# Optimization experiments

Hardware: AMD Instinct MI355X
Metric: run time of the kernel (lower is better)

## Reference

```python
import jax, jax.numpy as jnp
import numpy as np
from jax import lax

INPUT_DIM = 16
H1, H2 = 64, 32
OUT_DIM = 1
B, T = 4096, 168


def _uniform(key, shape, k):
    return jax.random.uniform(key, shape, jnp.float32, -k, k)


def setup_inputs() -> dict:
    key = jax.random.key(0)
    ks = jax.random.split(key, 12)
    k1 = 1.0 / np.sqrt(H1)
    k2 = 1.0 / np.sqrt(H2)
    return {
        "x": jax.random.normal(ks[0], (B, T, INPUT_DIM), jnp.float32),
        # layer 1 (PyTorch gate order: i, f, g, o)
        "W_ih1": _uniform(ks[1], (4 * H1, INPUT_DIM), k1),
        "W_hh1": _uniform(ks[2], (4 * H1, H1), k1),
        "b_ih1": _uniform(ks[3], (4 * H1,), k1),
        "b_hh1": _uniform(ks[4], (4 * H1,), k1),
        # layer 2
        "W_ih2": _uniform(ks[5], (4 * H2, H1), k2),
        "W_hh2": _uniform(ks[6], (4 * H2, H2), k2),
        "b_ih2": _uniform(ks[7], (4 * H2,), k2),
        "b_hh2": _uniform(ks[8], (4 * H2,), k2),
        # final linear
        "W_fc": _uniform(ks[9], (OUT_DIM, H2), k2),
        "b_fc": _uniform(ks[10], (OUT_DIM,), k2),
    }


def _lstm(x, W_ih, W_hh, b_ih, b_hh, hidden):
    # Precompute input-to-gate projections for all timesteps: [B, T, 4H]
    xg = jnp.einsum("btd,gd->btg", x, W_ih) + b_ih + b_hh

    def step(carry, xt):
        h, c = carry
        gates = xt + h @ W_hh.T  # [B, 4H]
        i, f, g, o = jnp.split(gates, 4, axis=-1)
        i = jax.nn.sigmoid(i)
        f = jax.nn.sigmoid(f)
        g = jnp.tanh(g)
        o = jax.nn.sigmoid(o)
        c = f * c + i * g
        h = o * jnp.tanh(c)
        return (h, c), h

    bsz = x.shape[0]
    init = (jnp.zeros((bsz, hidden), x.dtype), jnp.zeros((bsz, hidden), x.dtype))
    (_, _), hs = lax.scan(step, init, jnp.swapaxes(xg, 0, 1))  # hs: [T, B, H]
    return jnp.swapaxes(hs, 0, 1)  # [B, T, H]


def reference(x, W_ih1, W_hh1, b_ih1, b_hh1, W_ih2, W_hh2, b_ih2, b_hh2, W_fc, b_fc):
    # Dropout layers are identity at inference (p=0.2 in train only).
    h1 = _lstm(x, W_ih1, W_hh1, b_ih1, b_hh1, H1)   # [B, T, 64]
    h2 = _lstm(h1, W_ih2, W_hh2, b_ih2, b_hh2, H2)  # [B, T, 32]
    last = h2[:, -1, :]                              # [B, 32]
    return last @ W_fc.T + b_fc                      # [B, OUT_DIM]
```

## Files before the change

### kernel.cpp

```cpp
#include <hip/hip_runtime.h>


typedef __bf16 bf16x8 __attribute__((ext_vector_type(8)));
typedef float  f32x4  __attribute__((ext_vector_type(4)));

constexpr int T_SEQ = 168;
constexpr int NB    = 16;

__device__ __forceinline__ void split_bf16(float x, __bf16& hi, __bf16& lo) {
  hi = (__bf16)x;
  lo = (__bf16)(x - (float)hi);
}

__device__ __forceinline__ void split_fast(float x, __bf16& hi, __bf16& lo) {
  const unsigned u  = __float_as_uint(x);
  const unsigned hb = u & 0xFFFF0000u;
  const float    lf = x - __uint_as_float(hb);
  hi = __builtin_bit_cast(__bf16, (unsigned short)(hb >> 16));
  lo = __builtin_bit_cast(__bf16, (unsigned short)(__float_as_uint(lf) >> 16));
}

__device__ __forceinline__ void load_frag8(const float* __restrict__ Wrow, int k0,
                                           bf16x8& hi, bf16x8& lo) {
#pragma unroll
  for (int j = 0; j < 8; ++j) {
    float v = Wrow[k0 + j];
    __bf16 h = (__bf16)v;
    hi[j] = h;
    lo[j] = (__bf16)(v - (float)h);
  }
}

#define MFMA(a, b, c) __builtin_amdgcn_mfma_f32_16x16x32_bf16((a), (b), (c), 0, 0, 0)

__global__ __launch_bounds__(512) __attribute__((amdgpu_waves_per_eu(2, 2)))
void lstm_mfma_kernel(const float* __restrict__ x,
    const float* __restrict__ Wih1, const float* __restrict__ Whh1,
    const float* __restrict__ bih1, const float* __restrict__ bhh1,
    const float* __restrict__ Wih2, const float* __restrict__ Whh2,
    const float* __restrict__ bih2, const float* __restrict__ bhh2,
    const float* __restrict__ Wfc,  const float* __restrict__ bfc,
    float* __restrict__ out)
{
  __shared__ __align__(16) __bf16 sA1[2][4 * 64 * 8];
  __shared__ __align__(16) __bf16 sA2[2][2 * 64 * 8];
  __shared__ __align__(16) __bf16 sW2lo[8 * 2 * 64 * 8];
  __shared__ __align__(16) float  sP[2][2 * 4 * 64 * 4];
  __shared__ __align__(16) float  sH2f[16 * 32];

  const int tid  = threadIdx.x;
  const int w    = tid >> 6;
  const int lane = tid & 63;
  const int q    = lane >> 4;
  const int col  = lane & 15;
  const int b0   = blockIdx.x * NB;

  const bool isL1  = (w < 4);
  const bool isL2b = (w == 4) || (w == 5);
  const bool isL2a = (w >= 6);
  const int  wl2b  = w - 4;
  const int  wl2a  = w - 6;

  if (isL1) __builtin_amdgcn_s_setprio(1);

  bf16x8 bhh[4][4];
  bf16x8 bih[4];
  f32x4  b1sd[4];
  if (isL1) {
#pragma unroll
    for (int g = 0; g < 4; ++g) {
      const int r = g * 64 + w * 16 + col;
      const float* Wr = Whh1 + r * 64;
      bf16x8 h0, l0, h1f, l1f;
      load_frag8(Wr, 0 * 32 + q * 8, h0, l0);
      load_frag8(Wr, 1 * 32 + q * 8, h1f, l1f);
      bhh[g][0] = h0; bhh[g][1] = h1f; bhh[g][2] = l0; bhh[g][3] = l1f;
      bf16x8 xh, xl;
      load_frag8(Wih1 + r * 16, (q & 1) * 8, xh, xl);
      bih[g] = (q < 2) ? xh : xl;
      const float bv = bih1[r] + bhh1[r];
      b1sd[g][0] = bv; b1sd[g][1] = bv; b1sd[g][2] = bv; b1sd[g][3] = bv;
    }
  }
  bf16x8 wh2h[4], wh2l[4];
  f32x4  b2sd[4];
  if (isL2b) {
#pragma unroll
    for (int g = 0; g < 4; ++g) {
      const int r = g * 32 + wl2b * 16 + col;
      bf16x8 hh, ll;
      load_frag8(Whh2 + r * 32, q * 8, hh, ll);
      wh2h[g] = hh; wh2l[g] = ll;
      const float bv = bih2[r] + bhh2[r];
      b2sd[g][0] = bv; b2sd[g][1] = bv; b2sd[g][2] = bv; b2sd[g][3] = bv;
    }
  }
  bf16x8 w2ih[4][2];
  if (isL2a) {
#pragma unroll
    for (int g = 0; g < 4; ++g) {
      const int r = g * 32 + wl2a * 16 + col;
#pragma unroll
      for (int kb = 0; kb < 2; ++kb) {
        bf16x8 hh, ll;
        load_frag8(Wih2 + r * 64, kb * 32 + q * 8, hh, ll);
        w2ih[g][kb] = hh;
      }
    }
  }

  for (int idx = tid; idx < 8 * 2 * 64; idx += 512) {
    const int nt  = idx >> 7;
    const int kb2 = (idx >> 6) & 1;
    const int ln  = idx & 63;
    const int qq  = ln >> 4, cc = ln & 15;
    const int g   = nt >> 1, wv = nt & 1;
    const int r   = g * 32 + wv * 16 + cc;
    const int k0  = kb2 * 32 + qq * 8;
    bf16x8 hh, ll;
    load_frag8(Wih2 + r * 64, k0, hh, ll);
    *(bf16x8*)&sW2lo[((nt * 2 + kb2) * 64 + ln) * 8] = ll;
  }

  {
    bf16x8 z;
#pragma unroll
    for (int j = 0; j < 8; ++j) z[j] = (__bf16)0.f;
    for (int i = tid; i < 2 * 4 * 64; i += 512) *(bf16x8*)&sA1[0][i * 8] = z;
    for (int i = tid; i < 2 * 2 * 64; i += 512) *(bf16x8*)&sA2[0][i * 8] = z;
  }
  __syncthreads();

  const float* xbase = x + ((size_t)(b0 + col) * T_SEQ) * 16 + (q & 1) * 8;
  float4 xcA, xcB, xnA, xnB;
  if (isL1) {
    xcA = *(const float4*)(xbase + 0);
    xcB = *(const float4*)(xbase + 4);
  }

  float c1s[4] = {0.f, 0.f, 0.f, 0.f};
  float c2s[4] = {0.f, 0.f, 0.f, 0.f};
  const int uu   = w * 16 + col;
  const int uu2b = wl2b * 16 + col;

  const int kbh  = uu >> 5;
  const int lnb  = ((uu & 31) >> 3) * 16;
  const int jj   = uu & 7;
  const int lnb2 = ((uu2b & 31) >> 3) * 16;
  const int jj2  = uu2b & 7;

  const f32x4 z4 = {0.f, 0.f, 0.f, 0.f};

#define CELL_UPDATE(ai_, af_, ag_, ao_, cprev_, ccout_, hfout_) do {           \
    const float Ei_ = __expf(-(ai_));                                          \
    const float Ef_ = __expf(-(af_));                                          \
    const float Eg_ = __expf((ag_) + (ag_));                                   \
    const float Eo_ = __expf(-(ao_));                                          \
    const float t1_ = (1.f + Ei_) * (Eg_ + 1.f);                               \
    const float t2_ = 1.f + Ef_;                                               \
    const float num_ = fmaf((cprev_), t1_, (Eg_ - 1.f) * t2_);                 \
    const float cc_  = num_ * __builtin_amdgcn_rcpf(t1_ * t2_);                \
    (ccout_) = cc_;                                                            \
    const float Ec_ = __expf(fminf(cc_ + cc_, 60.f));                          \
    (hfout_) = (Ec_ - 1.f) * __builtin_amdgcn_rcpf((1.f + Eo_) * (Ec_ + 1.f)); \
  } while (0)

#define STEP(Pc, DO_L1, DO_XPRE, DO_L2A, DO_L2B, DO_H2F, TT) do {              \
    if ((DO_L1) && isL1) {                                                     \
      bf16x8 a1[4];                                                            \
      _Pragma("unroll")                                                        \
      for (int kb = 0; kb < 4; ++kb)                                           \
        a1[kb] = *(const bf16x8*)&sA1[(Pc)][(kb * 64 + lane) * 8];             \
      if (DO_XPRE) {                                                           \
        const float* xr = xbase + (size_t)((TT) + 1) * 16;                     \
        xnA = *(const float4*)(xr + 0);                                        \
        xnB = *(const float4*)(xr + 4);                                        \
      }                                                                        \
      const float xc[8] = {xcA.x, xcA.y, xcA.z, xcA.w, xcB.x, xcB.y, xcB.z, xcB.w}; \
      bf16x8 xh8, xl8;                                                         \
      _Pragma("unroll")                                                        \
      for (int j = 0; j < 8; ++j) {                                            \
        __bf16 h_, l_; split_fast(xc[j], h_, l_);                              \
        xh8[j] = h_; xl8[j] = l_;                                              \
      }                                                                        \
      const bf16x8 ax0 = (q < 2) ? xh8 : xl8;                                  \
      const bf16x8 ax1 = (q < 2) ? xl8 : xh8;                                  \
      f32x4 ca[4], cb[4];                                                      \
      _Pragma("unroll")                                                        \
      for (int g = 0; g < 4; ++g) {                                            \
        ca[g] = MFMA(ax0,   bih[g],    b1sd[g]);                               \
        ca[g] = MFMA(ax1,   bih[g],    ca[g]);                                 \
        ca[g] = MFMA(a1[0], bhh[g][0], ca[g]);                                 \
        ca[g] = MFMA(a1[1], bhh[g][1], ca[g]);                                 \
        cb[g] = MFMA(a1[2], bhh[g][0], z4);                                    \
        cb[g] = MFMA(a1[3], bhh[g][1], cb[g]);                                 \
        cb[g] = MFMA(a1[0], bhh[g][2], cb[g]);                                 \
        cb[g] = MFMA(a1[1], bhh[g][3], cb[g]);                                 \
      }                                                                        \
      _Pragma("unroll")                                                        \
      for (int r = 0; r < 4; ++r) {                                            \
        const float ai = ca[0][r] + cb[0][r];                                  \
        const float af = ca[1][r] + cb[1][r];                                  \
        const float ag = ca[2][r] + cb[2][r];                                  \
        const float ao = ca[3][r] + cb[3][r];                                  \
        float cc, hf;                                                          \
        CELL_UPDATE(ai, af, ag, ao, c1s[r], cc, hf);                           \
        c1s[r] = cc;                                                           \
        __bf16 hh_, hl_;                                                       \
        split_fast(hf, hh_, hl_);                                              \
        const int m = q * 4 + r;                                               \
        sA1[1 - (Pc)][((kbh * 64) + lnb + m) * 8 + jj]       = hh_;            \
        sA1[1 - (Pc)][(((2 + kbh) * 64) + lnb + m) * 8 + jj] = hl_;            \
      }                                                                        \
      if (DO_XPRE) { xcA = xnA; xcB = xnB; }                                   \
    }                                                                          \
    if ((DO_L2A) && isL2a) {                                                   \
      bf16x8 a2[4];                                                            \
      _Pragma("unroll")                                                        \
      for (int kb = 0; kb < 4; ++kb)                                           \
        a2[kb] = *(const bf16x8*)&sA1[(Pc)][(kb * 64 + lane) * 8];             \
      _Pragma("unroll")                                                        \
      for (int g = 0; g < 4; ++g) {                                            \
        const int nt = g * 2 + wl2a;                                           \
        const bf16x8 bb2 = *(const bf16x8*)&sW2lo[((nt * 2 + 0) * 64 + lane) * 8]; \
        const bf16x8 bb3 = *(const bf16x8*)&sW2lo[((nt * 2 + 1) * 64 + lane) * 8]; \
        f32x4 pa;                                                              \
        pa = MFMA(a2[0], w2ih[g][0], z4);                         \
        pa = MFMA(a2[1], w2ih[g][1], pa);                                      \
        pa = MFMA(a2[0], bb2, pa);                                \
        pa = MFMA(a2[1], bb3, pa);                                             \
        pa = MFMA(a2[2], w2ih[g][0], pa);                         \
        pa = MFMA(a2[3], w2ih[g][1], pa);                                      \
        *(f32x4*)&sP[(Pc)][((wl2a * 4 + g) * 64 + lane) * 4] = pa;             \
      }                                                                        \
    }                                                                          \
    if ((DO_L2B) && isL2b) {                                                   \
      const bf16x8 ah0 = *(const bf16x8*)&sA2[1 - (Pc)][(0 * 64 + lane) * 8];  \
      const bf16x8 ah1 = *(const bf16x8*)&sA2[1 - (Pc)][(1 * 64 + lane) * 8];  \
      f32x4 c2[4];                                                             \
      _Pragma("unroll")                                                        \
      for (int g = 0; g < 4; ++g) {                                            \
        c2[g] = MFMA(ah0, wh2h[g], b2sd[g]);                                   \
        c2[g] = MFMA(ah1, wh2h[g], c2[g]);                                     \
        c2[g] = MFMA(ah0, wh2l[g], c2[g]);                                     \
        c2[g] += *(const f32x4*)&sP[1 - (Pc)][((wl2b * 4 + g) * 64 + lane) * 4]; \
      }                                                                        \
      _Pragma("unroll")                                                        \
      for (int r = 0; r < 4; ++r) {                                            \
        float cc, hf;                                                          \
        CELL_UPDATE(c2[0][r], c2[1][r], c2[2][r], c2[3][r], c2s[r], cc, hf);   \
        c2s[r] = cc;                                                           \
        __bf16 hh_, hl_;                                                       \
        split_fast(hf, hh_, hl_);                                              \
        const int m = q * 4 + r;                                               \
        sA2[(Pc)][((0 * 64) + lnb2 + m) * 8 + jj2] = hh_;                      \
        sA2[(Pc)][((1 * 64) + lnb2 + m) * 8 + jj2] = hl_;                      \
        if (DO_H2F) sH2f[m * 32 + uu2b] = hf;                                  \
      }                                                                        \
    }                                                                          \
    __syncthreads();                                                           \
  } while (0)

  STEP(0, true,  true,  false, false, false, 0);
  STEP(1, true,  true,  true,  false, false, 1);
  for (int t = 2; t < 166; t += 2) {
    STEP(0, true, true, true, true, false, t);
    STEP(1, true, true, true, true, false, t + 1);
  }
  STEP(0, true,  true,  true,  true,  false, 166);
  STEP(1, true,  false, true,  true,  false, 167);
  STEP(0, false, false, true,  true,  false, 168);
  STEP(1, false, false, false, true,  true,  169);
#undef STEP
#undef CELL_UPDATE

  if (tid < NB) {
    float s = bfc[0];
#pragma unroll
    for (int j = 0; j < 32; ++j) s = fmaf(Wfc[j], sH2f[tid * 32 + j], s);
    out[b0 + tid] = s;
  }
}

extern "C" void kernel_launch(void* const* d_in, const int* in_sizes, int n_in,
                              void* d_out, int out_size, void* d_ws, size_t ws_size,
                              hipStream_t stream) {
  (void)in_sizes; (void)n_in; (void)out_size; (void)d_ws; (void)ws_size;
  const float* x    = (const float*)d_in[0];
  const float* Wih1 = (const float*)d_in[1];
  const float* Whh1 = (const float*)d_in[2];
  const float* bih1 = (const float*)d_in[3];
  const float* bhh1 = (const float*)d_in[4];
  const float* Wih2 = (const float*)d_in[5];
  const float* Whh2 = (const float*)d_in[6];
  const float* bih2 = (const float*)d_in[7];
  const float* bhh2 = (const float*)d_in[8];
  const float* Wfc  = (const float*)d_in[9];
  const float* bfc  = (const float*)d_in[10];
  float* out = (float*)d_out;

  hipLaunchKernelGGL(lstm_mfma_kernel, dim3(4096 / NB), dim3(512), 0, stream,
                     x, Wih1, Whh1, bih1, bhh1, Wih2, Whh2, bih2, bhh2, Wfc, bfc, out);
}
```

Baseline: 270.0 us.

## Move layer-1 input projection off critical path into layer-2 input waves

The layer-1 input projection (x_t·W_ih1 plus bias) moves off the layer-1 waves and onto the two layer-2 input-projection waves. Those waves compute it one step ahead into a double-buffered shared-memory array, and layer 1 reads the result as its accumulator seed. This takes two MFMAs per gate, the x split and the x global loads out of the serial recurrence chain on the layer-1 waves. In exchange, the L2a waves do more work per step and more shared memory is used, which could make them the new per-step bottleneck.

```diff
diff --git a/kernel.cpp b/kernel.cpp
--- a/kernel.cpp
+++ b/kernel.cpp
@@ -46,6 +46,7 @@
   __shared__ __align__(16) __bf16 sA2[2][2 * 64 * 8];
   __shared__ __align__(16) __bf16 sW2lo[8 * 2 * 64 * 8];
   __shared__ __align__(16) float  sP[2][2 * 4 * 64 * 4];
+  __shared__ __align__(16) float  sXg[2][16 * 64 * 4];
   __shared__ __align__(16) float  sH2f[16 * 32];
 
   const int tid  = threadIdx.x;
@@ -64,8 +65,6 @@
   if (isL1) __builtin_amdgcn_s_setprio(1);
 
   bf16x8 bhh[4][4];
-  bf16x8 bih[4];
-  f32x4  b1sd[4];
   if (isL1) {
 #pragma unroll
     for (int g = 0; g < 4; ++g) {
@@ -75,11 +74,6 @@
       load_frag8(Wr, 0 * 32 + q * 8, h0, l0);
       load_frag8(Wr, 1 * 32 + q * 8, h1f, l1f);
       bhh[g][0] = h0; bhh[g][1] = h1f; bhh[g][2] = l0; bhh[g][3] = l1f;
-      bf16x8 xh, xl;
-      load_frag8(Wih1 + r * 16, (q & 1) * 8, xh, xl);
-      bih[g] = (q < 2) ? xh : xl;
-      const float bv = bih1[r] + bhh1[r];
-      b1sd[g][0] = bv; b1sd[g][1] = bv; b1sd[g][2] = bv; b1sd[g][3] = bv;
     }
   }
   bf16x8 wh2h[4], wh2l[4];
@@ -96,6 +90,8 @@
     }
   }
   bf16x8 w2ih[4][2];
+  bf16x8 xw[8];
+  f32x4  xb[8];
   if (isL2a) {
 #pragma unroll
     for (int g = 0; g < 4; ++g) {
@@ -105,6 +101,20 @@
         bf16x8 hh, ll;
         load_frag8(Wih2 + r * 64, kb * 32 + q * 8, hh, ll);
         w2ih[g][kb] = hh;
+      }
+    }
+#pragma unroll
+    for (int pp = 0; pp < 2; ++pp) {
+#pragma unroll
+      for (int g = 0; g < 4; ++g) {
+        const int lw = wl2a * 2 + pp;
+        const int r  = g * 64 + lw * 16 + col;
+        bf16x8 hh, ll;
+        load_frag8(Wih1 + r * 16, (q & 1) * 8, hh, ll);
+        xw[pp * 4 + g] = (q < 2) ? hh : ll;
+        const float bv = bih1[r] + bhh1[r];
+        f32x4 s; s[0] = bv; s[1] = bv; s[2] = bv; s[3] = bv;
+        xb[pp * 4 + g] = s;
       }
     }
   }
@@ -129,14 +139,42 @@
     for (int i = tid; i < 2 * 4 * 64; i += 512) *(bf16x8*)&sA1[0][i * 8] = z;
     for (int i = tid; i < 2 * 2 * 64; i += 512) *(bf16x8*)&sA2[0][i * 8] = z;
   }
-  __syncthreads();
 
   const float* xbase = x + ((size_t)(b0 + col) * T_SEQ) * 16 + (q & 1) * 8;
   float4 xcA, xcB, xnA, xnB;
-  if (isL1) {
+
+#define XG_BODY(PDST, DO_PRE, TT) do {                                         \
+      const float xcv[8] = {xcA.x, xcA.y, xcA.z, xcA.w, xcB.x, xcB.y, xcB.z, xcB.w}; \
+      bf16x8 xh8, xl8;                                                         \
+      _Pragma("unroll")                                                        \
+      for (int j = 0; j < 8; ++j) {                                            \
+        __bf16 h_, l_; split_fast(xcv[j], h_, l_);                             \
+        xh8[j] = h_; xl8[j] = l_;                                              \
+      }                                                                        \
+      const bf16x8 ax0 = (q < 2) ? xh8 : xl8;                                  \
+      const bf16x8 ax1 = (q < 2) ? xl8 : xh8;                                  \
+      if (DO_PRE) {                                                            \
+        const float* xr = xbase + (size_t)((TT) + 2) * 16;                     \
+        xnA = *(const float4*)(xr + 0);                                        \
+        xnB = *(const float4*)(xr + 4);                                        \
+      }                                                                        \
+      _Pragma("unroll")                                                        \
+      for (int p = 0; p < 8; ++p) {                                            \
+        f32x4 pa = MFMA(ax0, xw[p], xb[p]);                                    \
+        pa = MFMA(ax1, xw[p], pa);                                             \
+        *(f32x4*)&sXg[(PDST)][(((wl2a * 2 + (p >> 2)) * 4 + (p & 3)) * 64 + lane) * 4] = pa; \
+      }                                                                        \
+      if (DO_PRE) { xcA = xnA; xcB = xnB; }                                    \
+  } while (0)
+
+  if (isL2a) {
     xcA = *(const float4*)(xbase + 0);
     xcB = *(const float4*)(xbase + 4);
-  }
+    XG_BODY(0, false, 0);
+    xcA = *(const float4*)(xbase + 16);
+    xcB = *(const float4*)(xbase + 20);
+  }
+  __syncthreads();
 
   float c1s[4] = {0.f, 0.f, 0.f, 0.f};
   float c2s[4] = {0.f, 0.f, 0.f, 0.f};
@@ -165,32 +203,20 @@
     (hfout_) = (Ec_ - 1.f) * __builtin_amdgcn_rcpf((1.f + Eo_) * (Ec_ + 1.f)); \
   } while (0)
 
-#define STEP(Pc, DO_L1, DO_XPRE, DO_L2A, DO_L2B, DO_H2F, TT) do {              \
+#define STEP(Pc, DO_L1, DO_XG, DO_XPRE, DO_L2A, DO_L2B, DO_H2F, TT) do {       \
     if ((DO_L1) && isL1) {                                                     \
+      f32x4 sd[4];                                                             \
+      _Pragma("unroll")                                                        \
+      for (int g = 0; g < 4; ++g)                                              \
+        sd[g] = *(const f32x4*)&sXg[(Pc)][((w * 4 + g) * 64 + lane) * 4];      \
       bf16x8 a1[4];                                                            \
       _Pragma("unroll")                                                        \
       for (int kb = 0; kb < 4; ++kb)                                           \
         a1[kb] = *(const bf16x8*)&sA1[(Pc)][(kb * 64 + lane) * 8];             \
-      if (DO_XPRE) {                                                           \
-        const float* xr = xbase + (size_t)((TT) + 1) * 16;                     \
-        xnA = *(const float4*)(xr + 0);                                        \
-        xnB = *(const float4*)(xr + 4);                                        \
-      }                                                                        \
-      const float xc[8] = {xcA.x, xcA.y, xcA.z, xcA.w, xcB.x, xcB.y, xcB.z, xcB.w}; \
-      bf16x8 xh8, xl8;                                                         \
-      _Pragma("unroll")                                                        \
-      for (int j = 0; j < 8; ++j) {                                            \
-        __bf16 h_, l_; split_fast(xc[j], h_, l_);                              \
-        xh8[j] = h_; xl8[j] = l_;                                              \
-      }                                                                        \
-      const bf16x8 ax0 = (q < 2) ? xh8 : xl8;                                  \
-      const bf16x8 ax1 = (q < 2) ? xl8 : xh8;                                  \
       f32x4 ca[4], cb[4];                                                      \
       _Pragma("unroll")                                                        \
       for (int g = 0; g < 4; ++g) {                                            \
-        ca[g] = MFMA(ax0,   bih[g],    b1sd[g]);                               \
-        ca[g] = MFMA(ax1,   bih[g],    ca[g]);                                 \
-        ca[g] = MFMA(a1[0], bhh[g][0], ca[g]);                                 \
+        ca[g] = MFMA(a1[0], bhh[g][0], sd[g]);                                 \
         ca[g] = MFMA(a1[1], bhh[g][1], ca[g]);                                 \
         cb[g] = MFMA(a1[2], bhh[g][0], z4);                                    \
         cb[g] = MFMA(a1[3], bhh[g][1], cb[g]);                                 \
@@ -212,26 +238,28 @@
         sA1[1 - (Pc)][((kbh * 64) + lnb + m) * 8 + jj]       = hh_;            \
         sA1[1 - (Pc)][(((2 + kbh) * 64) + lnb + m) * 8 + jj] = hl_;            \
       }                                                                        \
-      if (DO_XPRE) { xcA = xnA; xcB = xnB; }                                   \
     }                                                                          \
-    if ((DO_L2A) && isL2a) {                                                   \
-      bf16x8 a2[4];                                                            \
-      _Pragma("unroll")                                                        \
-      for (int kb = 0; kb < 4; ++kb)                                           \
-        a2[kb] = *(const bf16x8*)&sA1[(Pc)][(kb * 64 + lane) * 8];             \
-      _Pragma("unroll")                                                        \
-      for (int g = 0; g < 4; ++g) {                                            \
-        const int nt = g * 2 + wl2a;                                           \
-        const bf16x8 bb2 = *(const bf16x8*)&sW2lo[((nt * 2 + 0) * 64 + lane) * 8]; \
-        const bf16x8 bb3 = *(const bf16x8*)&sW2lo[((nt * 2 + 1) * 64 + lane) * 8]; \
-        f32x4 pa;                                                              \
-        pa = MFMA(a2[0], w2ih[g][0], z4);                         \
-        pa = MFMA(a2[1], w2ih[g][1], pa);                                      \
-        pa = MFMA(a2[0], bb2, pa);                                \
-        pa = MFMA(a2[1], bb3, pa);                                             \
-        pa = MFMA(a2[2], w2ih[g][0], pa);                         \
-        pa = MFMA(a2[3], w2ih[g][1], pa);                                      \
-        *(f32x4*)&sP[(Pc)][((wl2a * 4 + g) * 64 + lane) * 4] = pa;             \
+    if (isL2a) {                                                               \
+      if (DO_XG) XG_BODY(1 - (Pc), (DO_XPRE), TT);                             \
+      if (DO_L2A) {                                                            \
+        bf16x8 a2[4];                                                          \
+        _Pragma("unroll")                                                      \
+        for (int kb = 0; kb < 4; ++kb)                                         \
+          a2[kb] = *(const bf16x8*)&sA1[(Pc)][(kb * 64 + lane) * 8];           \
+        _Pragma("unroll")                                                      \
+        for (int g = 0; g < 4; ++g) {                                          \
+          const int nt = g * 2 + wl2a;                                         \
+          const bf16x8 bb2 = *(const bf16x8*)&sW2lo[((nt * 2 + 0) * 64 + lane) * 8]; \
+          const bf16x8 bb3 = *(const bf16x8*)&sW2lo[((nt * 2 + 1) * 64 + lane) * 8]; \
+          f32x4 pa;                                                            \
+          pa = MFMA(a2[0], w2ih[g][0], z4);                       \
+          pa = MFMA(a2[1], w2ih[g][1], pa);                                    \
+          pa = MFMA(a2[0], bb2, pa);                              \
+          pa = MFMA(a2[1], bb3, pa);                                           \
+          pa = MFMA(a2[2], w2ih[g][0], pa);                       \
+          pa = MFMA(a2[3], w2ih[g][1], pa);                                    \
+          *(f32x4*)&sP[(Pc)][((wl2a * 4 + g) * 64 + lane) * 4] = pa;           \
+        }                                                                      \
       }                                                                        \
     }                                                                          \
     if ((DO_L2B) && isL2b) {                                                   \
@@ -261,18 +289,19 @@
     __syncthreads();                                                           \
   } while (0)
 
-  STEP(0, true,  true,  false, false, false, 0);
-  STEP(1, true,  true,  true,  false, false, 1);
+  STEP(0, true,  true,  true,  false, false, false, 0);
+  STEP(1, true,  true,  true,  true,  false, false, 1);
   for (int t = 2; t < 166; t += 2) {
-    STEP(0, true, true, true, true, false, t);
-    STEP(1, true, true, true, true, false, t + 1);
-  }
-  STEP(0, true,  true,  true,  true,  false, 166);
-  STEP(1, true,  false, true,  true,  false, 167);
-  STEP(0, false, false, true,  true,  false, 168);
-  STEP(1, false, false, false, true,  true,  169);
+    STEP(0, true, true, true, true, true, false, t);
+    STEP(1, true, true, true, true, true, false, t + 1);
+  }
+  STEP(0, true,  true,  false, true,  true,  false, 166);
+  STEP(1, true,  false, false, true,  true,  false, 167);
+  STEP(0, false, false, false, true,  true,  false, 168);
+  STEP(1, false, false, false, false, true,  true,  169);
 #undef STEP
 #undef CELL_UPDATE
+#undef XG_BODY
 
   if (tid < NB) {
     float s = bfc[0];
```

New measurement: 419.5 us. 1.55x slower.
